# Optimization experiments

Measured on AMD Instinct MI355X. Metric: run time of the kernel, lower is better.

The kernel has to match this reference:

```python
import jax, jax.numpy as jnp
import numpy as np

C_IN = 512
OUT_CH = 256  # query/key gate channels
DIM = 64      # squeeze/extraction rank


def setup_inputs() -> dict:
    key = jax.random.key(0)
    ks = jax.random.split(key, 11)
    b, c, h, w = 16, C_IN, 64, 64

    def winit(k, o, i):
        # torch Conv2d default init: U(-s, s), s = 1/sqrt(fan_in)
        s = 1.0 / np.sqrt(i)
        return jax.random.uniform(k, (o, i), jnp.float32, -s, s)

    return {
        "x": jax.random.normal(ks[0], (b, c, h, w), jnp.float32),
        "Wq": winit(ks[1], OUT_CH, C_IN), "bq": winit(ks[2], OUT_CH, C_IN)[:, 0],
        "Wk": winit(ks[3], OUT_CH, C_IN), "bk": winit(ks[4], OUT_CH, C_IN)[:, 0],
        "Wv": winit(ks[5], C_IN, C_IN),   "bv": winit(ks[6], C_IN, C_IN)[:, 0],
        "Ws": winit(ks[7], DIM, C_IN),    "bs": winit(ks[8], DIM, C_IN)[:, 0],
        "We": winit(ks[9], DIM, C_IN),    "be": winit(ks[10], DIM, C_IN)[:, 0],
    }


def reference(x, Wq, bq, Wk, bk, Wv, bv, Ws, bs, We, be):
    b, c, h, w = x.shape
    n = h * w
    xf = x.reshape(b, c, n)  # [b, 512, n] (1x1 conv == matmul over channels)

    Q = jnp.einsum('oc,bcn->bon', Wq, xf) + bq[:, None]   # [b, 256, n]
    K = jnp.einsum('oc,bcn->bon', Wk, xf) + bk[:, None]   # [b, 256, n]
    gate = jax.nn.sigmoid(jnp.mean(Q * K, axis=1, keepdims=True))  # [b, 1, n]

    V = jnp.einsum('oc,bcn->bon', Wv, xf) + bv[:, None]   # [b, 512, n]
    V_dw = V * gate                                        # [b, 512, n]

    Qs = jnp.einsum('oc,bcn->bon', Ws, xf) + bs[:, None]   # [b, 64, n]
    Ke = jnp.einsum('oc,bcn->bon', We, xf) + be[:, None]   # [b, 64, n]

    energy = jnp.einsum('bcn,bdn->bcd', V_dw, Qs)           # [b, 512, 64]
    attention = jax.nn.softmax(energy, axis=-1)
    Vout = jnp.einsum('bcd,bdn->bcn', attention, Ke)        # [b, 512, n]

    return x + Vout.reshape(b, c, h, w)
```

## Files before the change

kernel.cpp:

```cpp
#include <hip/hip_runtime.h>

#define BATCH 16
#define CIN 512
#define NPIX 4096

typedef __attribute__((ext_vector_type(8))) short bf16x8;
typedef __attribute__((ext_vector_type(4))) float f32x4;

#define MFMA(a,b,c) __builtin_amdgcn_mfma_f32_16x16x32_bf16((a),(b),(c),0,0,0)

union PK  { short s[8]; bf16x8 v; };
union PK4 { short s[4]; uint2 u; };

__device__ __forceinline__ unsigned short bf16_rne(float f){
  unsigned u = __float_as_uint(f);
  return (unsigned short)((u + 0x7fffu + ((u >> 16) & 1u)) >> 16);
}
__device__ __forceinline__ void f32_split(float f, short &h, short &l){
  unsigned short hu = bf16_rne(f);
  h = (short)hu;
  float fh = __uint_as_float((unsigned)hu << 16);
  l = (short)bf16_rne(f - fh);
}
__device__ __forceinline__ void split8(float4 a, float4 b, bf16x8 &h, bf16x8 &l){
  float vv[8] = {a.x,a.y,a.z,a.w,b.x,b.y,b.z,b.w};
  PK ph, pl;
  #pragma unroll
  for (int z=0;z<8;z++){ short hh,ll; f32_split(vv[z],hh,ll); ph.s[z]=hh; pl.s[z]=ll; }
  h = ph.v; l = pl.v;
}

__device__ __forceinline__ int offBig(int row, int k){
  int s = k >> 3;
  s = (s & ~7) | ((s ^ row) & 7);
  return row*512 + s*8 + (k & 7);
}

__global__ __launch_bounds__(256)
void k_convw(const float* __restrict__ Wq, const float* __restrict__ bq,
             const float* __restrict__ Wk, const float* __restrict__ bk,
             const float* __restrict__ Ws, const float* __restrict__ bs,
             const float* __restrict__ We, const float* __restrict__ be,
             short* __restrict__ WG, short* __restrict__ WSE, short* __restrict__ WSL,
             float* __restrict__ BG, float* __restrict__ BSE){
  int t = blockIdx.x*256 + threadIdx.x;
  if (t < 512*512){
    int r = t >> 9, c = t & 511, o = r >> 1;
    float v = (r & 1) ? Wk[o*512+c] : Wq[o*512+c];
    WG[t] = (short)bf16_rne(v);
  }
  if (t < 128*512){
    int r = t >> 9, c = t & 511;
    float v = (r < 64) ? Ws[r*512+c] : We[(r-64)*512+c];
    short h,l; f32_split(v,h,l);
    WSE[t] = h;
    if (r < 64) WSL[t] = l;
  }
  if (t < 512) BG[t] = (t&1) ? bk[t>>1] : bq[t>>1];
  if (t < 128) BSE[t] = (t < 64) ? bs[t] : be[t-64];
}

__global__ __launch_bounds__(512, 4)
void k_front(const float* __restrict__ x, const short* __restrict__ WG,
             const float* __restrict__ BG, const short* __restrict__ WSE,
             const short* __restrict__ WSL, const float* __restrict__ BSE,
             float* __restrict__ QSG, short* __restrict__ KET, float* __restrict__ S){
  __shared__ __align__(16) short XS[64*512];
  __shared__ float QKf[512];
  __shared__ float GF[64];
  int nt = blockIdx.x, b = blockIdx.y;
  int n0 = nt*64;
  int tid = threadIdx.x, w = tid>>6, lane = tid&63;
  int lr = lane&15, lk = (lane>>4)<<3;

  {
    const float* xp = x + ((size_t)b*CIN + tid)*NPIX + n0;
    float4 vv[16];
    #pragma unroll
    for (int i=0;i<16;i++) vv[i] = *(const float4*)(xp + i*4);
    #pragma unroll
    for (int i=0;i<16;i++){
      float f[4] = {vv[i].x, vv[i].y, vv[i].z, vv[i].w};
      #pragma unroll
      for (int u=0;u<4;u++)
        XS[offBig(i*4+u, tid)] = (short)bf16_rne(f[u]);
    }
  }
  __syncthreads();

  int rq = (lane>>4)<<2;

  {
    const short* wgb = WG + (size_t)(w*64 + lr)*512 + lk;
    f32x4 acc[4][4] = {};
    for (int kt=0; kt<16; kt++){
      bf16x8 av[4];
      #pragma unroll
      for (int r=0;r<4;r++) av[r] = *(const bf16x8*)(wgb + r*16*512 + kt*32);
      bf16x8 bb[4];
      #pragma unroll
      for (int j=0;j<4;j++) bb[j] = *(const bf16x8*)&XS[offBig(j*16+lr, kt*32+lk)];
      #pragma unroll
      for (int r=0;r<4;r++)
        #pragma unroll
        for (int j=0;j<4;j++)
          acc[r][j] = MFMA(av[r], bb[j], acc[r][j]);
    }
    float p[4] = {0.f,0.f,0.f,0.f};
    #pragma unroll
    for (int r=0;r<4;r++){
      f32x4 bg = *(const f32x4*)&BG[w*64 + r*16 + rq];
      #pragma unroll
      for (int j=0;j<4;j++){
        f32x4 a4 = acc[r][j];
        p[j] += (a4[0]+bg[0])*(a4[1]+bg[1]) + (a4[2]+bg[2])*(a4[3]+bg[3]);
      }
    }
    #pragma unroll
    for (int j=0;j<4;j++){ p[j] += __shfl_xor(p[j],16); p[j] += __shfl_xor(p[j],32); }
    if (lane < 16){
      #pragma unroll
      for (int j=0;j<4;j++) QKf[w*64 + j*16 + lane] = p[j];
    }
  }
  __syncthreads();
  if (tid < 64){
    float s = 0.f;
    #pragma unroll
    for (int ww=0;ww<8;ww++) s += QKf[ww*64 + tid];
    GF[tid] = 1.f/(1.f + __expf(-s*(1.f/256.f)));
  }
  __syncthreads();

  bool isQs = (w < 4);
  const short* wb  = WSE + (size_t)((isQs ? (w*16) : (64 + (w-4)*16)) + lr)*512 + lk;
  const short* wlb = WSL + (size_t)((isQs ? (w*16) : 0) + lr)*512 + lk;
  f32x4 acc2[4] = {};
  for (int kt=0; kt<16; kt++){
    bf16x8 bb[4];
    #pragma unroll
    for (int j=0;j<4;j++) bb[j] = *(const bf16x8*)&XS[offBig(j*16+lr, kt*32+lk)];
    bf16x8 ah = *(const bf16x8*)(wb + kt*32);
    if (isQs){
      bf16x8 al = *(const bf16x8*)(wlb + kt*32);
      #pragma unroll
      for (int j=0;j<4;j++){
        acc2[j] = MFMA(al, bb[j], acc2[j]);
        acc2[j] = MFMA(ah, bb[j], acc2[j]);
      }
    } else {
      #pragma unroll
      for (int j=0;j<4;j++)
        acc2[j] = MFMA(ah, bb[j], acc2[j]);
    }
  }

  if (isQs){
    int row0 = w*16 + rq;
    f32x4 bs4 = *(const f32x4*)&BSE[row0];
    float srow[4] = {0.f,0.f,0.f,0.f};
    #pragma unroll
    for (int j=0;j<4;j++){
      int nl = j*16 + lr;
      float g = GF[nl];
      int n = n0 + nl;
      #pragma unroll
      for (int q=0;q<4;q++){
        float v = (acc2[j][q] + bs4[q]) * g;
        QSG[((size_t)(b*64) + row0 + q)*NPIX + n] = v;
        srow[q] += v;
      }
    }
    #pragma unroll
    for (int q=0;q<4;q++){
      float v = srow[q];
      v += __shfl_xor(v,1); v += __shfl_xor(v,2);
      v += __shfl_xor(v,4); v += __shfl_xor(v,8);
      if (lr == 0) atomicAdd(&S[b*64 + row0 + q], v);
    }
  } else {
    int d0 = (w-4)*16 + rq;
    f32x4 be4 = *(const f32x4*)&BSE[64 + d0];
    #pragma unroll
    for (int j=0;j<4;j++){
      int n = n0 + j*16 + lr;
      PK4 pk;
      #pragma unroll
      for (int q=0;q<4;q++) pk.s[q] = (short)bf16_rne(acc2[j][q] + be4[q]);
      *(uint2*)&KET[((size_t)(b*NPIX) + n)*64 + d0] = pk.u;
    }
  }
}

__global__ __launch_bounds__(512)
void k_M(const float* __restrict__ x, const float* __restrict__ QSG,
         float* __restrict__ M){
  int slab = blockIdx.x, b = blockIdx.y;
  int tid = threadIdx.x, w = tid>>6, lane = tid&63;
  int lr = lane&15, lk8 = (lane>>4)<<3;
  f32x4 acc[4][4] = {};
  for (int kt=0; kt<8; kt++){
    int noff = slab*256 + kt*32 + lk8;
    bf16x8 bh[4], bl[4];
    #pragma unroll
    for (int j=0;j<4;j++){
      const float* qp = QSG + ((size_t)(b*64) + j*16 + lr)*NPIX + noff;
      split8(*(const float4*)qp, *(const float4*)(qp+4), bh[j], bl[j]);
    }
    #pragma unroll
    for (int r=0;r<4;r++){
      const float* xp = x + ((size_t)(b*CIN) + w*64 + r*16 + lr)*NPIX + noff;
      bf16x8 ah, al;
      split8(*(const float4*)xp, *(const float4*)(xp+4), ah, al);
      #pragma unroll
      for (int j=0;j<4;j++){
        acc[r][j] = MFMA(al, bh[j], acc[r][j]);
        acc[r][j] = MFMA(ah, bl[j], acc[r][j]);
        acc[r][j] = MFMA(ah, bh[j], acc[r][j]);
      }
    }
  }
  int rq = (lane>>4)<<2;
  #pragma unroll
  for (int r=0;r<4;r++)
    #pragma unroll
    for (int j=0;j<4;j++)
      #pragma unroll
      for (int q=0;q<4;q++)
        atomicAdd(&M[((size_t)(b*CIN) + w*64 + r*16 + rq + q)*64 + j*16 + lr], acc[r][j][q]);
}

__global__ __launch_bounds__(256)
void k_energy(const float* __restrict__ Wv, const float* __restrict__ bv,
              const float* __restrict__ M, const float* __restrict__ S,
              float* __restrict__ EN){
  __shared__ __align__(16) float ML[128*68];
  int cch = blockIdx.x, b = blockIdx.y;
  int tid = threadIdx.x;
  int d4 = tid & 15, ci = tid >> 4;
  f32x4 acc[2] = {};
  for (int kt=0; kt<4; kt++){
    __syncthreads();
    for (int i = tid; i < 2048; i += 256){
      int k = i >> 4, c4 = (i & 15) * 4;
      *(float4*)&ML[k*68 + c4] = *(const float4*)&M[((size_t)(b*CIN) + kt*128 + k)*64 + c4];
    }
    __syncthreads();
    #pragma unroll
    for (int m=0;m<2;m++){
      int c = cch*32 + ci + 16*m;
      const float* wvp = Wv + (size_t)c*512 + kt*128;
      for (int k4=0;k4<32;k4++){
        float4 wv4 = *(const float4*)(wvp + k4*4);
        f32x4 m0 = *(const f32x4*)&ML[(k4*4+0)*68 + d4*4];
        f32x4 m1 = *(const f32x4*)&ML[(k4*4+1)*68 + d4*4];
        f32x4 m2 = *(const f32x4*)&ML[(k4*4+2)*68 + d4*4];
        f32x4 m3 = *(const f32x4*)&ML[(k4*4+3)*68 + d4*4];
        acc[m] += m0*wv4.x + m1*wv4.y + m2*wv4.z + m3*wv4.w;
      }
    }
  }
  f32x4 s4 = *(const f32x4*)&S[b*64 + d4*4];
  #pragma unroll
  for (int m=0;m<2;m++){
    int c = cch*32 + ci + 16*m;
    f32x4 r = acc[m] + s4*bv[c];
    *(f32x4*)&EN[((size_t)(b*CIN) + c)*64 + d4*4] = r;
  }
}

__global__ __launch_bounds__(256)
void k_softmax(const float* __restrict__ EN, short* __restrict__ ATT){
  int row = blockIdx.x*4 + (threadIdx.x>>6);
  int lane = threadIdx.x & 63;
  float v = EN[(size_t)row*64 + lane];
  float m = v;
  #pragma unroll
  for (int s=1;s<64;s<<=1) m = fmaxf(m, __shfl_xor(m, s));
  float e = __expf(v - m);
  float sum = e;
  #pragma unroll
  for (int s=1;s<64;s<<=1) sum += __shfl_xor(sum, s);
  ATT[(size_t)row*64 + lane] = (short)bf16_rne(e / sum);
}

__global__ __launch_bounds__(512)
void k_out(const float* __restrict__ x, const short* __restrict__ ATT,
           const short* __restrict__ KET, float* __restrict__ out){
  int nt = blockIdx.x, b = blockIdx.y;
  int n0 = nt*64;
  int tid = threadIdx.x, w = tid>>6, lane = tid&63;
  int lr = lane&15, lk = (lane>>4)<<3;
  f32x4 acc[4][4] = {};
  #pragma unroll
  for (int kt=0; kt<2; kt++){
    bf16x8 bb[4];
    #pragma unroll
    for (int j=0;j<4;j++)
      bb[j] = *(const bf16x8*)&KET[((size_t)(b*NPIX) + n0 + j*16 + lr)*64 + kt*32 + lk];
    #pragma unroll
    for (int r=0;r<4;r++){
      bf16x8 a = *(const bf16x8*)&ATT[((size_t)(b*CIN) + w*64 + r*16 + lr)*64 + kt*32 + lk];
      #pragma unroll
      for (int j=0;j<4;j++)
        acc[r][j] = MFMA(a, bb[j], acc[r][j]);
    }
  }
  int rq = (lane>>4)<<2;
  #pragma unroll
  for (int r=0;r<4;r++)
    #pragma unroll
    for (int j=0;j<4;j++){
      int col = n0 + j*16 + lr;
      #pragma unroll
      for (int q=0;q<4;q++){
        size_t idx = ((size_t)(b*CIN) + w*64 + r*16 + rq + q)*NPIX + col;
        out[idx] = x[idx] + acc[r][j][q];
      }
    }
}

extern "C" void kernel_launch(void* const* d_in, const int* in_sizes, int n_in,
                              void* d_out, int out_size, void* d_ws, size_t ws_size,
                              hipStream_t stream){
  const float* x   = (const float*)d_in[0];
  const float* Wq  = (const float*)d_in[1];
  const float* bq  = (const float*)d_in[2];
  const float* Wk  = (const float*)d_in[3];
  const float* bk  = (const float*)d_in[4];
  const float* Wv  = (const float*)d_in[5];
  const float* bv  = (const float*)d_in[6];
  const float* Wsq = (const float*)d_in[7];
  const float* bsq = (const float*)d_in[8];
  const float* We  = (const float*)d_in[9];
  const float* be  = (const float*)d_in[10];
  float* out = (float*)d_out;

  char* wsb = (char*)d_ws;
  size_t off = 0;
  auto alloc = [&](size_t bytes)->void*{
    void* p = wsb + off; off += (bytes + 255) & ~(size_t)255; return p;
  };
  short* WG   = (short*)alloc((size_t)512*512*2);
  short* WSE  = (short*)alloc((size_t)128*512*2);
  short* WSL  = (short*)alloc((size_t)64*512*2);
  float* BG   = (float*)alloc(512*4);
  float* BSE  = (float*)alloc(128*4);
  float* QSG  = (float*)alloc((size_t)BATCH*64*NPIX*4);
  short* KET  = (short*)alloc((size_t)BATCH*NPIX*64*2);
  float* Mb   = (float*)alloc((size_t)BATCH*512*64*4);
  float* Sb   = (float*)alloc((size_t)BATCH*64*4);
  float* EN   = (float*)alloc((size_t)BATCH*512*64*4);
  short* ATT  = (short*)alloc((size_t)BATCH*512*64*2);

  hipMemsetAsync(Mb, 0, (size_t)BATCH*512*64*4, stream);
  hipMemsetAsync(Sb, 0, (size_t)BATCH*64*4, stream);

  k_convw  <<<1024, 256, 0, stream>>>(Wq,bq,Wk,bk,Wsq,bsq,We,be, WG,WSE,WSL,BG,BSE);
  k_front  <<<dim3(64,16), 512, 0, stream>>>(x, WG, BG, WSE, WSL, BSE, QSG, KET, Sb);
  k_M      <<<dim3(16,16), 512, 0, stream>>>(x, QSG, Mb);
  k_energy <<<dim3(16,16), 256, 0, stream>>>(Wv, bv, Mb, Sb, EN);
  k_softmax<<<2048, 256, 0, stream>>>(EN, ATT);
  k_out    <<<dim3(64,16), 512, 0, stream>>>(x, ATT, KET, out);
}
```

Before: 269.9 us.

## Fuse front GEMMs into one pass with double-buffered LDS weight staging

Merges the Q/K gate GEMM and the Qs/Ke GEMM in k_front into a single K loop over a combined 640-row weight matrix. Weights are pre-tiled and swizzled per k-slice and streamed into LDS with global_load_lds double buffering, replacing per-lane global weight loads. Each wave now owns 80 output rows. This reads X from LDS once instead of twice and overlaps weight fetch with MFMA. The cost is much larger LDS use (about 150KB), which lowers occupancy to about 1 block per CU, and the extra lo-part MFMAs land unevenly across waves.

```diff
diff --git a/kernel.cpp b/kernel.cpp
--- a/kernel.cpp
+++ b/kernel.cpp
@@ -8,6 +8,10 @@
 typedef __attribute__((ext_vector_type(4))) float f32x4;
 
 #define MFMA(a,b,c) __builtin_amdgcn_mfma_f32_16x16x32_bf16((a),(b),(c),0,0,0)
+
+#define GLOAD(g, l) __builtin_amdgcn_global_load_lds( \
+    (const __attribute__((address_space(1))) unsigned int*)(g), \
+    (__attribute__((address_space(3))) unsigned int*)(l), 16, 0, 0)
 
 union PK  { short s[8]; bf16x8 v; };
 union PK4 { short s[4]; uint2 u; };
@@ -41,30 +45,33 @@
              const float* __restrict__ Wk, const float* __restrict__ bk,
              const float* __restrict__ Ws, const float* __restrict__ bs,
              const float* __restrict__ We, const float* __restrict__ be,
-             short* __restrict__ WG, short* __restrict__ WSE, short* __restrict__ WSL,
+             short* __restrict__ WALL, short* __restrict__ WLOT,
              float* __restrict__ BG, float* __restrict__ BSE){
   int t = blockIdx.x*256 + threadIdx.x;
-  if (t < 512*512){
-    int r = t >> 9, c = t & 511, o = r >> 1;
-    float v = (r & 1) ? Wk[o*512+c] : Wq[o*512+c];
-    WG[t] = (short)bf16_rne(v);
-  }
-  if (t < 128*512){
-    int r = t >> 9, c = t & 511;
-    float v = (r < 64) ? Ws[r*512+c] : We[(r-64)*512+c];
-    short h,l; f32_split(v,h,l);
-    WSE[t] = h;
-    if (r < 64) WSL[t] = l;
-  }
-  if (t < 512) BG[t] = (t&1) ? bk[t>>1] : bq[t>>1];
+  if (t < 640*512){
+    int r = t >> 9, k = t & 511;
+    float v = (r < 512) ? ((r & 1) ? Wk[(r>>1)*512 + k] : Wq[(r>>1)*512 + k])
+            : (r < 576) ? Ws[(r-512)*512 + k] : We[(r-576)*512 + k];
+    short h, l; f32_split(v, h, l);
+    int kt = k >> 5, lc = (k >> 3) & 3, e = k & 7;
+    int pc = lc ^ (r & 3);
+    WALL[((size_t)kt*640 + r)*32 + pc*8 + e] = h;
+    if (r >= 512 && r < 576){
+      int rlo = r - 512;
+      WLOT[((size_t)kt*64 + rlo)*32 + (lc ^ (rlo & 3))*8 + e] = l;
+    }
+  }
+  if (t < 512) BG[t] = (t & 1) ? bk[t>>1] : bq[t>>1];
   if (t < 128) BSE[t] = (t < 64) ? bs[t] : be[t-64];
 }
 
-__global__ __launch_bounds__(512, 4)
-void k_front(const float* __restrict__ x, const short* __restrict__ WG,
-             const float* __restrict__ BG, const short* __restrict__ WSE,
-             const short* __restrict__ WSL, const float* __restrict__ BSE,
+__global__ __launch_bounds__(512, 2)
+void k_front(const float* __restrict__ x, const short* __restrict__ WALL,
+             const short* __restrict__ WLOT, const float* __restrict__ BG,
+             const float* __restrict__ BSE,
              float* __restrict__ QSG, short* __restrict__ KET, float* __restrict__ S){
+  __shared__ __align__(16) short AB[2][640*32];
+  __shared__ __align__(16) short LO[2][64*32];
   __shared__ __align__(16) short XS[64*512];
   __shared__ float QKf[512];
   __shared__ float GF[64];
@@ -72,6 +79,18 @@
   int n0 = nt*64;
   int tid = threadIdx.x, w = tid>>6, lane = tid&63;
   int lr = lane&15, lk = (lane>>4)<<3;
+  int cg = lane>>4;
+
+  {
+    const char* src = (const char*)WALL;
+    #pragma unroll
+    for (int i=0;i<5;i++){
+      int slot = i*8 + w;
+      GLOAD(src + slot*1024 + lane*16, ((char*)&AB[0][0]) + slot*1024);
+    }
+    if (w < 4)
+      GLOAD((const char*)WLOT + w*1024 + lane*16, ((char*)&LO[0][0]) + w*1024);
+  }
 
   {
     const float* xp = x + ((size_t)b*CIN + tid)*NPIX + n0;
@@ -86,34 +105,58 @@
         XS[offBig(i*4+u, tid)] = (short)bf16_rne(f[u]);
     }
   }
-  __syncthreads();
+
+  f32x4 acc[5][4] = {};
+  int rowBase = w*80;
+
+  for (int kt=0; kt<16; kt++){
+    int cur = kt & 1;
+    __syncthreads();
+    if (kt < 15){
+      const char* src = (const char*)WALL + (size_t)(kt+1)*40960;
+      #pragma unroll
+      for (int i=0;i<5;i++){
+        int slot = i*8 + w;
+        GLOAD(src + slot*1024 + lane*16, ((char*)&AB[cur^1][0]) + slot*1024);
+      }
+      if (w < 4)
+        GLOAD((const char*)WLOT + (size_t)(kt+1)*4096 + w*1024 + lane*16,
+              ((char*)&LO[cur^1][0]) + w*1024);
+    }
+    bf16x8 bb[4];
+    #pragma unroll
+    for (int j=0;j<4;j++)
+      bb[j] = *(const bf16x8*)&XS[offBig(j*16+lr, kt*32+lk)];
+    int swz = ((cg ^ (lr & 3)) << 3);
+    #pragma unroll
+    for (int r=0;r<5;r++){
+      int rowL = rowBase + r*16 + lr;
+      bf16x8 a = *(const bf16x8*)&AB[cur][rowL*32 + swz];
+      #pragma unroll
+      for (int j=0;j<4;j++) acc[r][j] = MFMA(a, bb[j], acc[r][j]);
+      int F = w*5 + r;
+      if (F >= 32 && F < 36){
+        int rowLo = F*16 - 512 + lr;
+        bf16x8 alo = *(const bf16x8*)&LO[cur][rowLo*32 + swz];
+        #pragma unroll
+        for (int j=0;j<4;j++) acc[r][j] = MFMA(alo, bb[j], acc[r][j]);
+      }
+    }
+  }
 
   int rq = (lane>>4)<<2;
-
   {
-    const short* wgb = WG + (size_t)(w*64 + lr)*512 + lk;
-    f32x4 acc[4][4] = {};
-    for (int kt=0; kt<16; kt++){
-      bf16x8 av[4];
-      #pragma unroll
-      for (int r=0;r<4;r++) av[r] = *(const bf16x8*)(wgb + r*16*512 + kt*32);
-      bf16x8 bb[4];
-      #pragma unroll
-      for (int j=0;j<4;j++) bb[j] = *(const bf16x8*)&XS[offBig(j*16+lr, kt*32+lk)];
-      #pragma unroll
-      for (int r=0;r<4;r++)
+    float p[4] = {0.f,0.f,0.f,0.f};
+    #pragma unroll
+    for (int r=0;r<5;r++){
+      int F = w*5 + r;
+      if (F < 32){
+        f32x4 bg = *(const f32x4*)&BG[F*16 + rq];
         #pragma unroll
-        for (int j=0;j<4;j++)
-          acc[r][j] = MFMA(av[r], bb[j], acc[r][j]);
-    }
-    float p[4] = {0.f,0.f,0.f,0.f};
-    #pragma unroll
-    for (int r=0;r<4;r++){
-      f32x4 bg = *(const f32x4*)&BG[w*64 + r*16 + rq];
-      #pragma unroll
-      for (int j=0;j<4;j++){
-        f32x4 a4 = acc[r][j];
-        p[j] += (a4[0]+bg[0])*(a4[1]+bg[1]) + (a4[2]+bg[2])*(a4[3]+bg[3]);
+        for (int j=0;j<4;j++){
+          f32x4 a4 = acc[r][j];
+          p[j] += (a4[0]+bg[0])*(a4[1]+bg[1]) + (a4[2]+bg[2])*(a4[3]+bg[3]);
+        }
       }
     }
     #pragma unroll
@@ -132,62 +175,43 @@
   }
   __syncthreads();
 
-  bool isQs = (w < 4);
-  const short* wb  = WSE + (size_t)((isQs ? (w*16) : (64 + (w-4)*16)) + lr)*512 + lk;
-  const short* wlb = WSL + (size_t)((isQs ? (w*16) : 0) + lr)*512 + lk;
-  f32x4 acc2[4] = {};
-  for (int kt=0; kt<16; kt++){
-    bf16x8 bb[4];
-    #pragma unroll
-    for (int j=0;j<4;j++) bb[j] = *(const bf16x8*)&XS[offBig(j*16+lr, kt*32+lk)];
-    bf16x8 ah = *(const bf16x8*)(wb + kt*32);
-    if (isQs){
-      bf16x8 al = *(const bf16x8*)(wlb + kt*32);
+  #pragma unroll
+  for (int r=0;r<5;r++){
+    int F = w*5 + r;
+    if (F >= 32 && F < 36){
+      int row0 = F*16 - 512 + rq;
+      f32x4 bs4 = *(const f32x4*)&BSE[row0];
+      float srow[4] = {0.f,0.f,0.f,0.f};
       #pragma unroll
       for (int j=0;j<4;j++){
-        acc2[j] = MFMA(al, bb[j], acc2[j]);
-        acc2[j] = MFMA(ah, bb[j], acc2[j]);
-      }
-    } else {
-      #pragma unroll
-      for (int j=0;j<4;j++)
-        acc2[j] = MFMA(ah, bb[j], acc2[j]);
-    }
-  }
-
-  if (isQs){
-    int row0 = w*16 + rq;
-    f32x4 bs4 = *(const f32x4*)&BSE[row0];
-    float srow[4] = {0.f,0.f,0.f,0.f};
-    #pragma unroll
-    for (int j=0;j<4;j++){
-      int nl = j*16 + lr;
-      float g = GF[nl];
-      int n = n0 + nl;
+        int nl = j*16 + lr;
+        float g = GF[nl];
+        int n = n0 + nl;
+        #pragma unroll
+        for (int q=0;q<4;q++){
+          float v = (acc[r][j][q] + bs4[q]) * g;
+          QSG[((size_t)(b*64) + row0 + q)*NPIX + n] = v;
+          srow[q] += v;
+        }
+      }
       #pragma unroll
       for (int q=0;q<4;q++){
-        float v = (acc2[j][q] + bs4[q]) * g;
-        QSG[((size_t)(b*64) + row0 + q)*NPIX + n] = v;
-        srow[q] += v;
-      }
-    }
-    #pragma unroll
-    for (int q=0;q<4;q++){
-      float v = srow[q];
-      v += __shfl_xor(v,1); v += __shfl_xor(v,2);
-      v += __shfl_xor(v,4); v += __shfl_xor(v,8);
-      if (lr == 0) atomicAdd(&S[b*64 + row0 + q], v);
-    }
-  } else {
-    int d0 = (w-4)*16 + rq;
-    f32x4 be4 = *(const f32x4*)&BSE[64 + d0];
-    #pragma unroll
-    for (int j=0;j<4;j++){
-      int n = n0 + j*16 + lr;
-      PK4 pk;
-      #pragma unroll
-      for (int q=0;q<4;q++) pk.s[q] = (short)bf16_rne(acc2[j][q] + be4[q]);
-      *(uint2*)&KET[((size_t)(b*NPIX) + n)*64 + d0] = pk.u;
+        float v = srow[q];
+        v += __shfl_xor(v,1); v += __shfl_xor(v,2);
+        v += __shfl_xor(v,4); v += __shfl_xor(v,8);
+        if (lr == 0) atomicAdd(&S[b*64 + row0 + q], v);
+      }
+    } else if (F >= 36){
+      int d0 = F*16 - 576 + rq;
+      f32x4 be4 = *(const f32x4*)&BSE[64 + d0];
+      #pragma unroll
+      for (int j=0;j<4;j++){
+        int n = n0 + j*16 + lr;
+        PK4 pk;
+        #pragma unroll
+        for (int q=0;q<4;q++) pk.s[q] = (short)bf16_rne(acc[r][j][q] + be4[q]);
+        *(uint2*)&KET[((size_t)(b*NPIX) + n)*64 + d0] = pk.u;
+      }
     }
   }
 }
@@ -341,9 +365,8 @@
   auto alloc = [&](size_t bytes)->void*{
     void* p = wsb + off; off += (bytes + 255) & ~(size_t)255; return p;
   };
-  short* WG   = (short*)alloc((size_t)512*512*2);
-  short* WSE  = (short*)alloc((size_t)128*512*2);
-  short* WSL  = (short*)alloc((size_t)64*512*2);
+  short* WALL = (short*)alloc((size_t)640*512*2);
+  short* WLOT = (short*)alloc((size_t)64*512*2);
   float* BG   = (float*)alloc(512*4);
   float* BSE  = (float*)alloc(128*4);
   float* QSG  = (float*)alloc((size_t)BATCH*64*NPIX*4);
@@ -356,8 +379,8 @@
   hipMemsetAsync(Mb, 0, (size_t)BATCH*512*64*4, stream);
   hipMemsetAsync(Sb, 0, (size_t)BATCH*64*4, stream);
 
-  k_convw  <<<1024, 256, 0, stream>>>(Wq,bq,Wk,bk,Wsq,bsq,We,be, WG,WSE,WSL,BG,BSE);
-  k_front  <<<dim3(64,16), 512, 0, stream>>>(x, WG, BG, WSE, WSL, BSE, QSG, KET, Sb);
+  k_convw  <<<1280, 256, 0, stream>>>(Wq,bq,Wk,bk,Wsq,bsq,We,be, WALL,WLOT,BG,BSE);
+  k_front  <<<dim3(64,16), 512, 0, stream>>>(x, WALL, WLOT, BG, BSE, QSG, KET, Sb);
   k_M      <<<dim3(16,16), 512, 0, stream>>>(x, QSG, Mb);
   k_energy <<<dim3(16,16), 256, 0, stream>>>(Wv, bv, Mb, Sb, EN);
   k_softmax<<<2048, 256, 0, stream>>>(EN, ATT);
```

Measured after the change: 278.8 us. +3.3%, slower.
